# Optimization experiments

Measured on AMD Instinct MI355X. Metric: run time of the kernel, lower is better.

Reference implementation:

```python
import jax, jax.numpy as jnp
import numpy as np
import math

B, S, E, H = 2, 2048, 1024, 16
D = E // H  # head_dim = 64
WINDOW = 512
EPS = 1e-5


def _layernorm(x, gamma, beta):
    mu = jnp.mean(x, axis=-1, keepdims=True)
    var = jnp.var(x, axis=-1, keepdims=True)
    return (x - mu) * jax.lax.rsqrt(var + EPS) * gamma + beta


def setup_inputs() -> dict:
    key = jax.random.key(0)
    ks = jax.random.split(key, 5)
    return {
        "x": jax.random.normal(ks[0], (B, S, E), jnp.float32),
        "W_qkv": jax.random.normal(ks[1], (E, 3 * E), jnp.float32) * (E ** -0.5),
        "b_qkv": jax.random.normal(ks[2], (3 * E,), jnp.float32) * 0.02,
        "q_gamma": jnp.ones((D,), jnp.float32),
        "q_beta": jnp.zeros((D,), jnp.float32),
        "k_gamma": jnp.ones((D,), jnp.float32),
        "k_beta": jnp.zeros((D,), jnp.float32),
        "W_out": jax.random.normal(ks[3], (E, E), jnp.float32) * (E ** -0.5),
        "b_out": jax.random.normal(ks[4], (E,), jnp.float32) * 0.02,
    }


def reference(x, W_qkv, b_qkv, q_gamma, q_beta, k_gamma, k_beta, W_out, b_out):
    b, s, e = x.shape
    # fused QKV projection -> (3, B, H, S, D)
    qkv = (x @ W_qkv + b_qkv).reshape(b, s, 3, H, D).transpose(2, 0, 3, 1, 4)
    q, k, v = qkv[0], qkv[1], qkv[2]
    # qk_norm: LayerNorm over head_dim
    q = _layernorm(q, q_gamma, q_beta)
    k = _layernorm(k, k_gamma, k_beta)
    scores = jnp.einsum("bhqd,bhkd->bhqk", q, k) / math.sqrt(D)
    # causal + sliding-window mask (True = masked out)
    row = jnp.arange(s)[:, None]
    col = jnp.arange(s)[None, :]
    masked = (col > row) | (row - col >= WINDOW)  # sliding window subsumes causal
    scores = jnp.where(masked[None, None], -jnp.inf, scores)
    attn = jax.nn.softmax(scores, axis=-1)
    out = jnp.einsum("bhqk,bhkd->bhqd", attn, v)  # (B,H,S,D)
    out = out.transpose(0, 2, 1, 3).reshape(b, s, e)
    return out @ W_out + b_out
```

## Files before the change

kernel.cpp:

```cpp
#include <hip/hip_runtime.h>
#include <stdint.h>

typedef uint16_t u16;
typedef __attribute__((ext_vector_type(8))) short short8;
typedef __attribute__((ext_vector_type(4))) float f32x4;

#define DEV static __device__ __forceinline__

DEV u16 f2bf(float f) {
  uint32_t u = __float_as_uint(f);
  return (u16)((u + 0x7fffu + ((u >> 16) & 1u)) >> 16);
}
DEV float bf2f(u16 h) { return __uint_as_float(((uint32_t)h) << 16); }

DEV void gload16(const void* g, void* l) {
  __builtin_amdgcn_global_load_lds(
      (const __attribute__((address_space(1))) void*)g,
      (__attribute__((address_space(3))) void*)l, 16, 0, 0);
}

__global__ void k_cast4(const float* __restrict__ in, u16* __restrict__ out, int n4) {
  int i = blockIdx.x * blockDim.x + threadIdx.x;
  if (i >= n4) return;
  float4 v = ((const float4*)in)[i];
  uint2 p;
  p.x = (uint32_t)f2bf(v.x) | ((uint32_t)f2bf(v.y) << 16);
  p.y = (uint32_t)f2bf(v.z) | ((uint32_t)f2bf(v.w) << 16);
  ((uint2*)out)[i] = p;
}

__global__ void k_tcast(const float* __restrict__ Wm, u16* __restrict__ Wt, int K, int N) {
  __shared__ u16 t[64][65];
  int n0 = blockIdx.x * 64, k0 = blockIdx.y * 64;
  int tid = threadIdx.x;
#pragma unroll
  for (int i = 0; i < 16; ++i) {
    int idx = tid + i * 256, r = idx >> 6, c = idx & 63;
    t[r][c] = f2bf(Wm[(size_t)(k0 + r) * N + n0 + c]);
  }
  __syncthreads();
#pragma unroll
  for (int i = 0; i < 16; ++i) {
    int idx = tid + i * 256, r = idx >> 6, c = idx & 63;
    Wt[(size_t)(n0 + r) * K + k0 + c] = t[c][r];
  }
}

template <int OUT_BF16>
__global__ __launch_bounds__(256) void k_gemm4(
    const u16* __restrict__ A, const u16* __restrict__ Bt,
    const float* __restrict__ bias, void* __restrict__ Cout,
    int M, int N, int K) {
  __shared__ __attribute__((aligned(16))) u16 S[2][2][128 * 64];
  int bid = blockIdx.x;
  int ntn = N >> 7;
  int cpx = gridDim.x >> 3;
  int wg = (bid & 7) * cpx + (bid >> 3);
  int my = wg / ntn, nx = wg - my * ntn;
  int m0 = my * 128, n0 = nx * 128;
  int tid = threadIdx.x, lane = tid & 63, w = tid >> 6;
  int wr = (w >> 1) * 64, wc = (w & 1) * 64;
  int lr = lane & 15, lg = lane >> 4;
  int rsw = (lr & 7) << 3;
  int srow = tid >> 3;
  int scb = ((tid & 7) ^ ((tid >> 3) & 7)) * 8;
  f32x4 acc[4][4];
#pragma unroll
  for (int i = 0; i < 4; ++i)
#pragma unroll
    for (int j = 0; j < 4; ++j) acc[i][j] = (f32x4){0.f, 0.f, 0.f, 0.f};

  int nk = K >> 6;

#define STG4(buf, kt)                                                                   \
  do {                                                                                  \
    gload16(A + (size_t)(m0 + srow) * K + (kt) * 64 + scb, &S[buf][0][tid * 8]);        \
    gload16(A + (size_t)(m0 + 32 + srow) * K + (kt) * 64 + scb, &S[buf][0][2048 + tid * 8]);  \
    gload16(A + (size_t)(m0 + 64 + srow) * K + (kt) * 64 + scb, &S[buf][0][4096 + tid * 8]);  \
    gload16(A + (size_t)(m0 + 96 + srow) * K + (kt) * 64 + scb, &S[buf][0][6144 + tid * 8]);  \
    gload16(Bt + (size_t)(n0 + srow) * K + (kt) * 64 + scb, &S[buf][1][tid * 8]);       \
    gload16(Bt + (size_t)(n0 + 32 + srow) * K + (kt) * 64 + scb, &S[buf][1][2048 + tid * 8]); \
    gload16(Bt + (size_t)(n0 + 64 + srow) * K + (kt) * 64 + scb, &S[buf][1][4096 + tid * 8]); \
    gload16(Bt + (size_t)(n0 + 96 + srow) * K + (kt) * 64 + scb, &S[buf][1][6144 + tid * 8]); \
  } while (0)

  STG4(0, 0);
  asm volatile("s_waitcnt vmcnt(0)" ::: "memory");
  __syncthreads();

  for (int t = 0; t < nk; ++t) {
    int cur = t & 1;
    if (t + 1 < nk) STG4(cur ^ 1, t + 1);
#pragma unroll
    for (int ks = 0; ks < 2; ++ks) {
      short8 af[4], bf[4];
#pragma unroll
      for (int mi = 0; mi < 4; ++mi)
        af[mi] = *(const short8*)&S[cur][0][((wr + mi * 16 + lr) * 64 + ks * 32 + lg * 8) ^ rsw];
#pragma unroll
      for (int ni = 0; ni < 4; ++ni)
        bf[ni] = *(const short8*)&S[cur][1][((wc + ni * 16 + lr) * 64 + ks * 32 + lg * 8) ^ rsw];
      __builtin_amdgcn_s_setprio(1);
#pragma unroll
      for (int mi = 0; mi < 4; ++mi)
#pragma unroll
        for (int ni = 0; ni < 4; ++ni)
          acc[mi][ni] = __builtin_amdgcn_mfma_f32_16x16x32_bf16(af[mi], bf[ni], acc[mi][ni], 0, 0, 0);
      __builtin_amdgcn_s_setprio(0);
    }
    asm volatile("s_waitcnt vmcnt(0)" ::: "memory");
    __syncthreads();
  }
#undef STG4

  int rg = lg * 4;
#pragma unroll
  for (int mi = 0; mi < 4; ++mi) {
#pragma unroll
    for (int ni = 0; ni < 4; ++ni) {
      int col = n0 + wc + ni * 16 + lr;
      float bv = bias[col];
#pragma unroll
      for (int j = 0; j < 4; ++j) {
        int row = m0 + wr + mi * 16 + rg + j;
        float o = acc[mi][ni][j] + bv;
        if (OUT_BF16) ((u16*)Cout)[(size_t)row * N + col] = f2bf(o);
        else ((float*)Cout)[(size_t)row * N + col] = o;
      }
    }
  }
}

__global__ void k_lnsplit2(const u16* __restrict__ qkv,
                           const float* __restrict__ qg, const float* __restrict__ qb,
                           const float* __restrict__ kg, const float* __restrict__ kb,
                           u16* __restrict__ Qn, u16* __restrict__ Kn) {
  int wv = blockIdx.x * 4 + (threadIdx.x >> 6);
  int lane = threadIdx.x & 63;
  int p = wv * 2 + (lane >> 5);
  int ln32 = lane & 31;
  int h = p & 15, row = p >> 4;
  const u16* base = qkv + (size_t)row * 3072 + h * 64 + ln32 * 2;
  uint uq = *(const uint*)base;
  uint uk = *(const uint*)(base + 1024);
  float q0 = bf2f((u16)uq), q1 = bf2f((u16)(uq >> 16));
  float k0 = bf2f((u16)uk), k1 = bf2f((u16)(uk >> 16));
  float qs = q0 + q1, qs2 = q0 * q0 + q1 * q1;
  float ks = k0 + k1, ks2 = k0 * k0 + k1 * k1;
#pragma unroll
  for (int m = 16; m > 0; m >>= 1) {
    qs += __shfl_xor(qs, m, 64);
    qs2 += __shfl_xor(qs2, m, 64);
    ks += __shfl_xor(ks, m, 64);
    ks2 += __shfl_xor(ks2, m, 64);
  }
  float qm = qs * (1.f / 64), km = ks * (1.f / 64);
  float qv = qs2 * (1.f / 64) - qm * qm, kv = ks2 * (1.f / 64) - km * km;
  float qr = rsqrtf(qv + 1e-5f), kr = rsqrtf(kv + 1e-5f);
  float2 g2 = ((const float2*)qg)[ln32], b2 = ((const float2*)qb)[ln32];
  float2 kg2 = ((const float2*)kg)[ln32], kb2 = ((const float2*)kb)[ln32];
  int b = row >> 11, s = row & 2047;
  size_t o = ((size_t)(b * 16 + h) * 2048 + s) * 64 + ln32 * 2;
  const float QSCL = 0.125f * 1.44269504f;
  u16 oq0 = f2bf(((q0 - qm) * qr * g2.x + b2.x) * QSCL);
  u16 oq1 = f2bf(((q1 - qm) * qr * g2.y + b2.y) * QSCL);
  u16 ok0 = f2bf((k0 - km) * kr * kg2.x + kb2.x);
  u16 ok1 = f2bf((k1 - km) * kr * kg2.y + kb2.y);
  *(uint*)(Qn + o) = (uint)oq0 | ((uint)oq1 << 16);
  *(uint*)(Kn + o) = (uint)ok0 | ((uint)ok1 << 16);
}

__global__ void k_vt(const u16* __restrict__ qkv, u16* __restrict__ Vt) {
  __shared__ u16 t[64][66];
  int bid = blockIdx.x;
  int bh = bid & 31, st = bid >> 5;
  int b = bh >> 4, h = bh & 15;
  int s0 = st * 64;
  int tid = threadIdx.x;
#pragma unroll
  for (int i = 0; i < 16; ++i) {
    int idx = tid + i * 256, r = idx >> 6, c = idx & 63;
    t[r][c] = qkv[(size_t)(b * 2048 + s0 + r) * 3072 + 2048 + h * 64 + c];
  }
  __syncthreads();
#pragma unroll
  for (int i = 0; i < 16; ++i) {
    int idx = tid + i * 256, d = idx >> 6, s = idx & 63;
    Vt[((size_t)bh * 64 + d) * 2048 + s0 + s] = t[s][d];
  }
}

__global__ __launch_bounds__(256) void k_attn6(
    const u16* __restrict__ Qn, const u16* __restrict__ Kn,
    const u16* __restrict__ Vt, u16* __restrict__ attb) {
  __shared__ __attribute__((aligned(16))) u16 KL[2][4096];
  __shared__ __attribute__((aligned(16))) u16 VL[2][4096];
  __shared__ __attribute__((aligned(16))) u16 Pl[4][16 * 72];
  int bid = blockIdx.x;
  int xcd = bid & 7, idx = bid >> 3;
  int bh = xcd * 4 + (idx & 3);
  int qt = 31 - (idx >> 2);
  int q0 = qt * 64;
  int tid = threadIdx.x, lane = tid & 63, w = tid >> 6;
  int ln15 = lane & 15, lg = lane >> 4;
  int qlo = q0 + w * 16;
  const u16* Qh = Qn + (size_t)bh * (2048 * 64);
  const u16* Kh = Kn + (size_t)bh * (2048 * 64);
  const u16* Vh = Vt + (size_t)bh * (64 * 2048);
  int rsw = (ln15 & 7) << 3;
  int srow = tid >> 3;
  int scb = ((tid & 7) ^ ((tid >> 3) & 7)) * 8;

  short8 qf[2];
#pragma unroll
  for (int h2 = 0; h2 < 2; ++h2)
    qf[h2] = *(const short8*)(Qh + (size_t)(qlo + ln15) * 64 + h2 * 32 + lg * 8);

  f32x4 oacc[4];
#pragma unroll
  for (int dt = 0; dt < 4; ++dt) oacc[dt] = (f32x4){0.f, 0.f, 0.f, 0.f};
  float lwp[4] = {0.f, 0.f, 0.f, 0.f};

  int t0 = q0 >= 512 ? (q0 - 511) >> 6 : 0;
  int t1 = (q0 + 63) >> 6;

#define STAGE_A6(buf, kt)                                                              \
  do {                                                                                 \
    const u16* Kt_ = Kh + (size_t)(kt) * 4096;                                         \
    gload16(Kt_ + (size_t)srow * 64 + scb, &KL[buf][tid * 8]);                         \
    gload16(Kt_ + (size_t)(srow + 32) * 64 + scb, &KL[buf][2048 + tid * 8]);           \
    const u16* Vt_ = Vh + (size_t)(kt) * 64;                                           \
    gload16(Vt_ + (size_t)srow * 2048 + scb, &VL[buf][tid * 8]);                       \
    gload16(Vt_ + (size_t)(srow + 32) * 2048 + scb, &VL[buf][2048 + tid * 8]);         \
  } while (0)

  STAGE_A6(0, t0);
  asm volatile("s_waitcnt vmcnt(0)" ::: "memory");
  __syncthreads();

  for (int t = t0; t <= t1; ++t) {
    int cur = (t - t0) & 1;
    if (t + 1 <= t1) STAGE_A6(cur ^ 1, t + 1);
    int kt6 = t * 64;
    if (kt6 <= qlo + 15 && kt6 + 63 >= qlo - 511) {
      short8 kf[4][2];
#pragma unroll
      for (int c = 0; c < 4; ++c)
#pragma unroll
        for (int h2 = 0; h2 < 2; ++h2)
          kf[c][h2] = *(const short8*)&KL[cur][((c * 16 + ln15) * 64 + h2 * 32 + lg * 8) ^ rsw];
      f32x4 sf[4];
      __builtin_amdgcn_s_setprio(1);
#pragma unroll
      for (int c = 0; c < 4; ++c) {
        f32x4 z = (f32x4){0.f, 0.f, 0.f, 0.f};
        z = __builtin_amdgcn_mfma_f32_16x16x32_bf16(qf[0], kf[c][0], z, 0, 0, 0);
        sf[c] = __builtin_amdgcn_mfma_f32_16x16x32_bf16(qf[1], kf[c][1], z, 0, 0, 0);
      }
      __builtin_amdgcn_s_setprio(0);
      bool interior = (kt6 + 63 <= qlo) && (kt6 >= qlo - 496);
      if (interior) {
#pragma unroll
        for (int c = 0; c < 4; ++c)
#pragma unroll
          for (int j = 0; j < 4; ++j) {
            float p = __builtin_amdgcn_exp2f(sf[c][j]);
            sf[c][j] = p;
            lwp[j] += p;
          }
      } else {
#pragma unroll
        for (int c = 0; c < 4; ++c) {
          int kk = kt6 + c * 16 + ln15;
#pragma unroll
          for (int j = 0; j < 4; ++j) {
            int q = qlo + lg * 4 + j;
            bool msk = (kk > q) || ((q - kk) >= 512);
            float p = __builtin_amdgcn_exp2f(msk ? -1e30f : sf[c][j]);
            sf[c][j] = p;
            lwp[j] += p;
          }
        }
      }
#pragma unroll
      for (int c = 0; c < 4; ++c)
#pragma unroll
        for (int j = 0; j < 4; ++j) {
          uint32_t u = __float_as_uint(sf[c][j]);
          Pl[w][(lg * 4 + j) * 72 + c * 16 + ln15] = (u16)((u + 0x8000u) >> 16);
        }
      short8 vf[4][2];
#pragma unroll
      for (int dt = 0; dt < 4; ++dt)
#pragma unroll
        for (int h2 = 0; h2 < 2; ++h2)
          vf[dt][h2] = *(const short8*)&VL[cur][((dt * 16 + ln15) * 64 + h2 * 32 + lg * 8) ^ rsw];
      __builtin_amdgcn_s_setprio(1);
#pragma unroll
      for (int h2 = 0; h2 < 2; ++h2) {
        short8 pf = *(const short8*)&Pl[w][ln15 * 72 + h2 * 32 + lg * 8];
#pragma unroll
        for (int dt = 0; dt < 4; ++dt)
          oacc[dt] = __builtin_amdgcn_mfma_f32_16x16x32_bf16(pf, vf[dt][h2], oacc[dt], 0, 0, 0);
      }
      __builtin_amdgcn_s_setprio(0);
    }
    asm volatile("s_waitcnt vmcnt(0)" ::: "memory");
    __syncthreads();
  }
#undef STAGE_A6

  int b = bh >> 4, hh = bh & 15;
#pragma unroll
  for (int j = 0; j < 4; ++j) {
    float rs = lwp[j];
#pragma unroll
    for (int m = 8; m > 0; m >>= 1) rs += __shfl_xor(rs, m, 64);
    float inv = rs > 0.f ? 1.f / rs : 0.f;
    int row = b * 2048 + qlo + lg * 4 + j;
#pragma unroll
    for (int dt = 0; dt < 4; ++dt)
      attb[(size_t)row * 1024 + hh * 64 + dt * 16 + ln15] = f2bf(oacc[dt][j] * inv);
  }
}

extern "C" void kernel_launch(void* const* d_in, const int* in_sizes, int n_in,
                              void* d_out, int out_size, void* d_ws, size_t ws_size,
                              hipStream_t stream) {
  const float* x = (const float*)d_in[0];
  const float* Wqkv = (const float*)d_in[1];
  const float* bqkv = (const float*)d_in[2];
  const float* qg = (const float*)d_in[3];
  const float* qb = (const float*)d_in[4];
  const float* kg = (const float*)d_in[5];
  const float* kb = (const float*)d_in[6];
  const float* Wout = (const float*)d_in[7];
  const float* bout = (const float*)d_in[8];
  float* out = (float*)d_out;

  char* ws = (char*)d_ws;
  u16* qkvb = (u16*)(ws);
  u16* attb = (u16*)(ws);
  u16* Qn = (u16*)(ws + 25165824);
  u16* Kn = (u16*)(ws + 33554432);
  u16* xb = (u16*)(ws + 41943040);
  u16* Vt = xb;
  u16* wqkvT = (u16*)(ws + 50331648);
  u16* woutT = (u16*)(ws + 56623104);

  k_cast4<<<4096, 256, 0, stream>>>(x, xb, 4194304 / 4);
  k_tcast<<<dim3(48, 16), 256, 0, stream>>>(Wqkv, wqkvT, 1024, 3072);
  k_tcast<<<dim3(16, 16), 256, 0, stream>>>(Wout, woutT, 1024, 1024);
  k_gemm4<1><<<768, 256, 0, stream>>>(xb, wqkvT, bqkv, qkvb, 4096, 3072, 1024);
  k_lnsplit2<<<8192, 256, 0, stream>>>(qkvb, qg, qb, kg, kb, Qn, Kn);
  k_vt<<<1024, 256, 0, stream>>>(qkvb, Vt);
  k_attn6<<<1024, 256, 0, stream>>>(Qn, Kn, Vt, attb);
  k_gemm4<0><<<256, 256, 0, stream>>>(attb, woutT, bout, out, 4096, 1024, 1024);
}
```

Baseline: 110.0 us.

## Fuse QK LayerNorm and V transpose into the QKV GEMM epilogue

Adds a dedicated QKV GEMM whose epilogue applies bias, per-head LayerNorm and the softmax scale for Q and K. It writes them straight into head-major layout, and writes V directly in transposed layout. This removes the bf16 qkv intermediate round trip and two kernel launches (lnsplit and V transpose). The cost is a heavier epilogue with cross-lane shuffles and scattered 2-byte stores for Q and K, which may coalesce poorly.

```diff
diff --git a/kernel.cpp b/kernel.cpp
--- a/kernel.cpp
+++ b/kernel.cpp
@@ -43,6 +43,146 @@
   for (int i = 0; i < 16; ++i) {
     int idx = tid + i * 256, r = idx >> 6, c = idx & 63;
     Wt[(size_t)(n0 + r) * K + k0 + c] = t[c][r];
+  }
+}
+
+__global__ __launch_bounds__(256) void k_gemmqkv(
+    const u16* __restrict__ A, const u16* __restrict__ Bt,
+    const float* __restrict__ bias,
+    const float* __restrict__ qg, const float* __restrict__ qb,
+    const float* __restrict__ kg, const float* __restrict__ kb,
+    u16* __restrict__ Qn, u16* __restrict__ Kn, u16* __restrict__ Vt) {
+  const int K = 1024, N = 3072;
+  __shared__ __attribute__((aligned(16))) u16 S[2][2][128 * 64];
+  int bid = blockIdx.x;
+  int ntn = N >> 7;
+  int cpx = gridDim.x >> 3;
+  int wg = (bid & 7) * cpx + (bid >> 3);
+  int my = wg / ntn, nx = wg - my * ntn;
+  int m0 = my * 128, n0 = nx * 128;
+  int tid = threadIdx.x, lane = tid & 63, w = tid >> 6;
+  int wr = (w >> 1) * 64, wc = (w & 1) * 64;
+  int lr = lane & 15, lg = lane >> 4;
+  int rsw = (lr & 7) << 3;
+  int srow = tid >> 3;
+  int scb = ((tid & 7) ^ ((tid >> 3) & 7)) * 8;
+  f32x4 acc[4][4];
+#pragma unroll
+  for (int i = 0; i < 4; ++i)
+#pragma unroll
+    for (int j = 0; j < 4; ++j) acc[i][j] = (f32x4){0.f, 0.f, 0.f, 0.f};
+
+  int nk = K >> 6;
+
+#define STGQ(buf, kt)                                                                   \
+  do {                                                                                  \
+    gload16(A + (size_t)(m0 + srow) * K + (kt) * 64 + scb, &S[buf][0][tid * 8]);        \
+    gload16(A + (size_t)(m0 + 32 + srow) * K + (kt) * 64 + scb, &S[buf][0][2048 + tid * 8]);  \
+    gload16(A + (size_t)(m0 + 64 + srow) * K + (kt) * 64 + scb, &S[buf][0][4096 + tid * 8]);  \
+    gload16(A + (size_t)(m0 + 96 + srow) * K + (kt) * 64 + scb, &S[buf][0][6144 + tid * 8]);  \
+    gload16(Bt + (size_t)(n0 + srow) * K + (kt) * 64 + scb, &S[buf][1][tid * 8]);       \
+    gload16(Bt + (size_t)(n0 + 32 + srow) * K + (kt) * 64 + scb, &S[buf][1][2048 + tid * 8]); \
+    gload16(Bt + (size_t)(n0 + 64 + srow) * K + (kt) * 64 + scb, &S[buf][1][4096 + tid * 8]); \
+    gload16(Bt + (size_t)(n0 + 96 + srow) * K + (kt) * 64 + scb, &S[buf][1][6144 + tid * 8]); \
+  } while (0)
+
+  STGQ(0, 0);
+  asm volatile("s_waitcnt vmcnt(0)" ::: "memory");
+  __syncthreads();
+
+  for (int t = 0; t < nk; ++t) {
+    int cur = t & 1;
+    if (t + 1 < nk) STGQ(cur ^ 1, t + 1);
+#pragma unroll
+    for (int ks = 0; ks < 2; ++ks) {
+      short8 af[4], bf[4];
+#pragma unroll
+      for (int mi = 0; mi < 4; ++mi)
+        af[mi] = *(const short8*)&S[cur][0][((wr + mi * 16 + lr) * 64 + ks * 32 + lg * 8) ^ rsw];
+#pragma unroll
+      for (int ni = 0; ni < 4; ++ni)
+        bf[ni] = *(const short8*)&S[cur][1][((wc + ni * 16 + lr) * 64 + ks * 32 + lg * 8) ^ rsw];
+      __builtin_amdgcn_s_setprio(1);
+#pragma unroll
+      for (int mi = 0; mi < 4; ++mi)
+#pragma unroll
+        for (int ni = 0; ni < 4; ++ni)
+          acc[mi][ni] = __builtin_amdgcn_mfma_f32_16x16x32_bf16(af[mi], bf[ni], acc[mi][ni], 0, 0, 0);
+      __builtin_amdgcn_s_setprio(0);
+    }
+    asm volatile("s_waitcnt vmcnt(0)" ::: "memory");
+    __syncthreads();
+  }
+#undef STGQ
+
+  int rg = lg * 4;
+  int sec = n0 >> 10;
+  int hh = ((n0 + wc) >> 6) & 15;
+  int b = m0 >> 11;
+  int s0 = m0 & 2047;
+
+  if (sec < 2) {
+    const float* gp = sec ? kg : qg;
+    const float* bp = sec ? kb : qb;
+    float scl = sec ? 1.f : (0.125f * 1.44269504f);
+    u16* op = sec ? Kn : Qn;
+    float gv[4], bev[4], bb[4];
+#pragma unroll
+    for (int ni = 0; ni < 4; ++ni) {
+      int d = ni * 16 + lr;
+      gv[ni] = gp[d];
+      bev[ni] = bp[d];
+      bb[ni] = bias[n0 + wc + d];
+    }
+    size_t hb = (size_t)(b * 16 + hh) * 2048 * 64;
+#pragma unroll
+    for (int mi = 0; mi < 4; ++mi) {
+      float a[4][4], ps[4], ps2[4];
+#pragma unroll
+      for (int ni = 0; ni < 4; ++ni)
+#pragma unroll
+        for (int j = 0; j < 4; ++j) a[ni][j] = acc[mi][ni][j] + bb[ni];
+#pragma unroll
+      for (int j = 0; j < 4; ++j) {
+        ps[j] = a[0][j] + a[1][j] + a[2][j] + a[3][j];
+        ps2[j] = a[0][j] * a[0][j] + a[1][j] * a[1][j] + a[2][j] * a[2][j] + a[3][j] * a[3][j];
+      }
+#pragma unroll
+      for (int m = 1; m < 16; m <<= 1)
+#pragma unroll
+        for (int j = 0; j < 4; ++j) {
+          ps[j] += __shfl_xor(ps[j], m, 64);
+          ps2[j] += __shfl_xor(ps2[j], m, 64);
+        }
+#pragma unroll
+      for (int j = 0; j < 4; ++j) {
+        float mean = ps[j] * (1.f / 64);
+        float var = ps2[j] * (1.f / 64) - mean * mean;
+        float r = rsqrtf(var + 1e-5f);
+        int row = s0 + wr + mi * 16 + rg + j;
+        size_t base = hb + (size_t)row * 64;
+#pragma unroll
+        for (int ni = 0; ni < 4; ++ni) {
+          float v = ((a[ni][j] - mean) * r * gv[ni] + bev[ni]) * scl;
+          op[base + ni * 16 + lr] = f2bf(v);
+        }
+      }
+    }
+  } else {
+    u16* vbase = Vt + (size_t)(b * 16 + hh) * 64 * 2048;
+#pragma unroll
+    for (int ni = 0; ni < 4; ++ni) {
+      int d = ni * 16 + lr;
+      float bb = bias[n0 + wc + d];
+#pragma unroll
+      for (int mi = 0; mi < 4; ++mi) {
+        int row0 = s0 + wr + mi * 16 + rg;
+        uint2 pk;
+        pk.x = (uint32_t)f2bf(acc[mi][ni][0] + bb) | ((uint32_t)f2bf(acc[mi][ni][1] + bb) << 16);
+        pk.y = (uint32_t)f2bf(acc[mi][ni][2] + bb) | ((uint32_t)f2bf(acc[mi][ni][3] + bb) << 16);
+        *(uint2*)(vbase + (size_t)d * 2048 + row0) = pk;
+      }
+    }
   }
 }
 
@@ -128,65 +268,6 @@
         else ((float*)Cout)[(size_t)row * N + col] = o;
       }
     }
-  }
-}
-
-__global__ void k_lnsplit2(const u16* __restrict__ qkv,
-                           const float* __restrict__ qg, const float* __restrict__ qb,
-                           const float* __restrict__ kg, const float* __restrict__ kb,
-                           u16* __restrict__ Qn, u16* __restrict__ Kn) {
-  int wv = blockIdx.x * 4 + (threadIdx.x >> 6);
-  int lane = threadIdx.x & 63;
-  int p = wv * 2 + (lane >> 5);
-  int ln32 = lane & 31;
-  int h = p & 15, row = p >> 4;
-  const u16* base = qkv + (size_t)row * 3072 + h * 64 + ln32 * 2;
-  uint uq = *(const uint*)base;
-  uint uk = *(const uint*)(base + 1024);
-  float q0 = bf2f((u16)uq), q1 = bf2f((u16)(uq >> 16));
-  float k0 = bf2f((u16)uk), k1 = bf2f((u16)(uk >> 16));
-  float qs = q0 + q1, qs2 = q0 * q0 + q1 * q1;
-  float ks = k0 + k1, ks2 = k0 * k0 + k1 * k1;
-#pragma unroll
-  for (int m = 16; m > 0; m >>= 1) {
-    qs += __shfl_xor(qs, m, 64);
-    qs2 += __shfl_xor(qs2, m, 64);
-    ks += __shfl_xor(ks, m, 64);
-    ks2 += __shfl_xor(ks2, m, 64);
-  }
-  float qm = qs * (1.f / 64), km = ks * (1.f / 64);
-  float qv = qs2 * (1.f / 64) - qm * qm, kv = ks2 * (1.f / 64) - km * km;
-  float qr = rsqrtf(qv + 1e-5f), kr = rsqrtf(kv + 1e-5f);
-  float2 g2 = ((const float2*)qg)[ln32], b2 = ((const float2*)qb)[ln32];
-  float2 kg2 = ((const float2*)kg)[ln32], kb2 = ((const float2*)kb)[ln32];
-  int b = row >> 11, s = row & 2047;
-  size_t o = ((size_t)(b * 16 + h) * 2048 + s) * 64 + ln32 * 2;
-  const float QSCL = 0.125f * 1.44269504f;
-  u16 oq0 = f2bf(((q0 - qm) * qr * g2.x + b2.x) * QSCL);
-  u16 oq1 = f2bf(((q1 - qm) * qr * g2.y + b2.y) * QSCL);
-  u16 ok0 = f2bf((k0 - km) * kr * kg2.x + kb2.x);
-  u16 ok1 = f2bf((k1 - km) * kr * kg2.y + kb2.y);
-  *(uint*)(Qn + o) = (uint)oq0 | ((uint)oq1 << 16);
-  *(uint*)(Kn + o) = (uint)ok0 | ((uint)ok1 << 16);
-}
-
-__global__ void k_vt(const u16* __restrict__ qkv, u16* __restrict__ Vt) {
-  __shared__ u16 t[64][66];
-  int bid = blockIdx.x;
-  int bh = bid & 31, st = bid >> 5;
-  int b = bh >> 4, h = bh & 15;
-  int s0 = st * 64;
-  int tid = threadIdx.x;
-#pragma unroll
-  for (int i = 0; i < 16; ++i) {
-    int idx = tid + i * 256, r = idx >> 6, c = idx & 63;
-    t[r][c] = qkv[(size_t)(b * 2048 + s0 + r) * 3072 + 2048 + h * 64 + c];
-  }
-  __syncthreads();
-#pragma unroll
-  for (int i = 0; i < 16; ++i) {
-    int idx = tid + i * 256, d = idx >> 6, s = idx & 63;
-    Vt[((size_t)bh * 64 + d) * 2048 + s0 + s] = t[s][d];
   }
 }
 
@@ -339,21 +420,18 @@
   float* out = (float*)d_out;
 
   char* ws = (char*)d_ws;
-  u16* qkvb = (u16*)(ws);
   u16* attb = (u16*)(ws);
-  u16* Qn = (u16*)(ws + 25165824);
-  u16* Kn = (u16*)(ws + 33554432);
-  u16* xb = (u16*)(ws + 41943040);
-  u16* Vt = xb;
-  u16* wqkvT = (u16*)(ws + 50331648);
-  u16* woutT = (u16*)(ws + 56623104);
+  u16* Vt = (u16*)(ws + 8388608);
+  u16* Qn = (u16*)(ws + 16777216);
+  u16* Kn = (u16*)(ws + 25165824);
+  u16* xb = (u16*)(ws + 33554432);
+  u16* wqkvT = (u16*)(ws + 41943040);
+  u16* woutT = (u16*)(ws + 48234496);
 
   k_cast4<<<4096, 256, 0, stream>>>(x, xb, 4194304 / 4);
   k_tcast<<<dim3(48, 16), 256, 0, stream>>>(Wqkv, wqkvT, 1024, 3072);
   k_tcast<<<dim3(16, 16), 256, 0, stream>>>(Wout, woutT, 1024, 1024);
-  k_gemm4<1><<<768, 256, 0, stream>>>(xb, wqkvT, bqkv, qkvb, 4096, 3072, 1024);
-  k_lnsplit2<<<8192, 256, 0, stream>>>(qkvb, qg, qb, kg, kb, Qn, Kn);
-  k_vt<<<1024, 256, 0, stream>>>(qkvb, Vt);
+  k_gemmqkv<<<768, 256, 0, stream>>>(xb, wqkvT, bqkv, qg, qb, kg, kb, Qn, Kn, Vt);
   k_attn6<<<1024, 256, 0, stream>>>(Qn, Kn, Vt, attb);
   k_gemm4<0><<<256, 256, 0, stream>>>(attb, woutT, bout, out, 4096, 1024, 1024);
 }
```

After: 100.0 us. 1.1x faster.
